# Kernel tuning notes

Measured on AMD Instinct MI355X. Metric: run time of the kernel, lower is better.

The kernel has to match this reference:

```python
import jax, jax.numpy as jnp
import numpy as np

Z_DIM = 64
SEQ_LEN = 100
SEQ_DIM = 32
INPUT_SIZE = 128
H_ENC = 256
H_DEC = 256
BATCH = 2048


def setup_inputs() -> dict:
    key = jax.random.key(0)
    ks = jax.random.split(key, 26)
    w = lambda k, sh: jax.random.normal(k, sh, jnp.float32) * 0.05
    return {
        "x": jax.random.normal(ks[0], (BATCH, SEQ_LEN, SEQ_DIM), jnp.float32),
        "eps": jax.random.normal(ks[1], (BATCH, Z_DIM), jnp.float32),
        "W_ee": w(ks[2], (SEQ_DIM, INPUT_SIZE)), "b_ee": w(ks[3], (INPUT_SIZE,)),
        "Wih_f": w(ks[4], (INPUT_SIZE, 3 * H_ENC)), "Whh_f": w(ks[5], (H_ENC, 3 * H_ENC)),
        "bih_f": w(ks[6], (3 * H_ENC,)), "bhh_f": w(ks[7], (3 * H_ENC,)),
        "Wih_b": w(ks[8], (INPUT_SIZE, 3 * H_ENC)), "Whh_b": w(ks[9], (H_ENC, 3 * H_ENC)),
        "bih_b": w(ks[10], (3 * H_ENC,)), "bhh_b": w(ks[11], (3 * H_ENC,)),
        "W_enc": w(ks[12], (2 * H_ENC, 2 * Z_DIM)), "b_enc": w(ks[13], (2 * Z_DIM,)),
        "W_z2h": w(ks[14], (Z_DIM, H_DEC)), "b_z2h": w(ks[15], (H_DEC,)),
        "W_h2i": w(ks[16], (H_DEC, INPUT_SIZE // 2)), "b_h2i": w(ks[17], (INPUT_SIZE // 2,)),
        "Wih_d": w(ks[18], (INPUT_SIZE, 3 * H_DEC)), "Whh_d": w(ks[19], (H_DEC, 3 * H_DEC)),
        "bih_d": w(ks[20], (3 * H_DEC,)), "bhh_d": w(ks[21], (3 * H_DEC,)),
        "W_ed": w(ks[22], (SEQ_DIM, INPUT_SIZE // 2)), "b_ed": w(ks[23], (INPUT_SIZE // 2,)),
        "W_dec": w(ks[24], (H_DEC, SEQ_DIM)), "b_dec": w(ks[25], (SEQ_DIM,)),
    }


def _gru_cell(x, h, Wih, Whh, bih, bhh):
    # PyTorch GRU cell math (gate order: reset, update, new)
    gi = x @ Wih + bih
    gh = h @ Whh + bhh
    ir, iz, in_ = jnp.split(gi, 3, axis=-1)
    hr, hz, hn = jnp.split(gh, 3, axis=-1)
    r = jax.nn.sigmoid(ir + hr)
    u = jax.nn.sigmoid(iz + hz)
    n = jnp.tanh(in_ + r * hn)
    return (1.0 - u) * n + u * h


def reference(x, eps, W_ee, b_ee, Wih_f, Whh_f, bih_f, bhh_f, Wih_b, Whh_b, bih_b, bhh_b,
              W_enc, b_enc, W_z2h, b_z2h, W_h2i, b_h2i, Wih_d, Whh_d, bih_d, bhh_d,
              W_ed, b_ed, W_dec, b_dec):
    B = x.shape[0]
    # ---- encoder ----
    xe = jax.nn.relu(x @ W_ee + b_ee)  # [B, L, 128]
    h0 = jnp.zeros((B, H_ENC), x.dtype)

    def enc_step(h, xt):
        return _gru_cell(xt, h, Wih_f, Whh_f, bih_f, bhh_f), None

    h_fwd, _ = jax.lax.scan(enc_step, h0, xe.transpose(1, 0, 2))
    # backward direction: only its output at the LAST timestep is used by the
    # original (output[:, -1, :]), which equals a single GRU step on the last
    # input from the zero initial state -> identical math, no wasted scan.
    h_bwd = _gru_cell(xe[:, -1], h0, Wih_b, Whh_b, bih_b, bhh_b)
    stats = jnp.concatenate([h_fwd, h_bwd], axis=-1) @ W_enc + b_enc  # [B, 2z]
    mu, logvar = stats[:, :Z_DIM], stats[:, Z_DIM:]
    z = mu + jnp.exp(logvar * 0.5) * eps
    h_dec0 = jax.nn.relu(z @ W_z2h + b_z2h)           # initial hidden [B, 256]
    hid_inp = jax.nn.relu(h_dec0 @ W_h2i + b_h2i)     # [B, 64]
    cur = jax.nn.relu(jnp.zeros((B, SEQ_DIM), x.dtype) @ W_ed + b_ed)  # zero start token
    inp0 = jnp.concatenate([cur, hid_inp], axis=-1)   # [B, 128]

    def dec_step(carry, _):
        h, inp = carry
        h2 = _gru_cell(inp, h, Wih_d, Whh_d, bih_d, bhh_d)
        x_cur = h2 @ W_dec + b_dec                    # [B, SEQ_DIM]
        nxt = jnp.concatenate([jax.nn.relu(x_cur @ W_ed + b_ed),
                               jax.nn.relu(h2 @ W_h2i + b_h2i)], axis=-1)
        return (h2, nxt), x_cur

    _, xs = jax.lax.scan(dec_step, (h_dec0, inp0), None, length=SEQ_LEN)
    x_recon = xs.transpose(1, 0, 2)                   # [B, L, SEQ_DIM]
    return x_recon, mu, logvar
```

## Files before the change

### kernel.cpp

```cpp
#include <hip/hip_runtime.h>
#include <hip/hip_bf16.h>

typedef __bf16 bf16x8 __attribute__((ext_vector_type(8)));
typedef float  f32x4  __attribute__((ext_vector_type(4)));
typedef unsigned short u16;

#define DEVI __device__ __forceinline__
#define MFMA __builtin_amdgcn_mfma_f32_16x16x32_bf16

DEVI u16 f2bf(float f){
  unsigned u = __builtin_bit_cast(unsigned, f);
  u += 0x7fffu + ((u >> 16) & 1u);
  return (u16)(u >> 16);
}
DEVI float bf2f(u16 h){
  unsigned u = ((unsigned)h) << 16;
  return __builtin_bit_cast(float, u);
}

enum : int {
  OFF_IHF = 0,
  OFF_HHF = 196608,
  OFF_IHB = 589824,
  OFF_IHD = 786432,
  OFF_HHD = 983040,
  OFF_ENC = 1376256,
  OFF_Z2H = 1507328,
  OFF_H2I = 1540096,
  OFF_DEC = 1572864,
  OFF_EE  = 1589248,
  OFF_ED  = 1597440,
  OFF_DE  = 1601536,
  OFF_BDE = 1634304,
  WS_TOTAL = 1634560
};

DEVI void packseg(const float* __restrict__ W, u16* __restrict__ dst, int li, int N, int KT){
  int j = li & 7, l = (li >> 3) & 63, f = li >> 9;
  int kt = f % KT, ntg = f / KT;
  int k = kt * 32 + ((l >> 4) << 3) + j;
  int col = (ntg << 4) + (l & 15);
  dst[li] = f2bf(W[k * N + col]);
}

__global__ void pack_all(const float* Wihf, const float* Whhf, const float* Wihb,
                         const float* Wihd, const float* Whhd, const float* Wenc,
                         const float* Wz2h, const float* Wh2i, const float* Wdec,
                         const float* Wee,  const float* Wed,
                         const float* bed,  const float* bdec, char* ws)
{
  int idx = blockIdx.x * 256 + threadIdx.x;
  if (idx < 98304) { packseg(Wihf, (u16*)(ws+OFF_IHF), idx, 768, 4); return; } idx -= 98304;
  if (idx < 196608){ packseg(Whhf, (u16*)(ws+OFF_HHF), idx, 768, 8); return; } idx -= 196608;
  if (idx < 98304) { packseg(Wihb, (u16*)(ws+OFF_IHB), idx, 768, 4); return; } idx -= 98304;
  if (idx < 98304) { packseg(Wihd, (u16*)(ws+OFF_IHD), idx, 768, 4); return; } idx -= 98304;
  if (idx < 196608){ packseg(Whhd, (u16*)(ws+OFF_HHD), idx, 768, 8); return; } idx -= 196608;
  if (idx < 65536) { packseg(Wenc, (u16*)(ws+OFF_ENC), idx, 128, 16); return; } idx -= 65536;
  if (idx < 16384) { packseg(Wz2h, (u16*)(ws+OFF_Z2H), idx, 256, 2); return; } idx -= 16384;
  if (idx < 16384) { packseg(Wh2i, (u16*)(ws+OFF_H2I), idx, 64, 8); return; } idx -= 16384;
  if (idx < 8192)  { packseg(Wdec, (u16*)(ws+OFF_DEC), idx, 32, 8); return; } idx -= 8192;
  if (idx < 4096)  { packseg(Wee,  (u16*)(ws+OFF_EE),  idx, 128, 1); return; } idx -= 4096;
  if (idx < 2048)  { packseg(Wed,  (u16*)(ws+OFF_ED),  idx, 64, 1); return; } idx -= 2048;
  if (idx < 16384){
    int j = idx & 7, l = (idx >> 3) & 63, f = idx >> 9;
    int kt = f & 7, ntg = f >> 3;
    int k = kt * 32 + ((l >> 4) << 3) + j;
    int col = (ntg << 4) + (l & 15);
    float acc = 0.f;
    for (int m = 0; m < 32; ++m) acc += Wdec[k*32 + m] * Wed[m*64 + col];
    ((u16*)(ws+OFF_DE))[idx] = f2bf(acc);
    return;
  } idx -= 16384;
  if (idx < 64){
    float acc = bed[idx];
    for (int m = 0; m < 32; ++m) acc += bdec[m] * Wed[m*64 + idx];
    ((float*)(ws+OFF_BDE))[idx] = acc;
  }
}

enum : int { RB_A1 = 272, RB_A2 = 528, RB_X = 80 };

DEVI bf16x8 ldF(const char* buf, int row, int kElem, int rowB){
  return *(const bf16x8*)(buf + row * rowB + kElem * 2);
}
DEVI void stBf(char* buf, int row, int col, int rowB, float v){
  *(u16*)(buf + row * rowB + col * 2) = f2bf(v);
}
DEVI bf16x8 gfrag(const u16* P, int ntg, int KT, int kt, int l){
  return *(const bf16x8*)(P + ((size_t)(ntg * KT + kt) * 64 + l) * 8);
}

DEVI float sigm(float x){ return 1.0f / (1.0f + __expf(-x)); }
DEVI float tanh_f(float x){ return 1.0f - 2.0f / (1.0f + __expf(2.0f * x)); }

DEVI void stage_x(const float* __restrict__ xg, int s0, int t, char* Xb, int tid){
  if (tid < 256){
    int s = tid >> 4, d0 = (tid & 15) * 2;
    float2 v = *(const float2*)(xg + (size_t)(s0 + s) * 3200 + t * 32 + d0);
    unsigned pk = (unsigned)f2bf(v.x) | ((unsigned)f2bf(v.y) << 16);
    *(unsigned*)(Xb + s * RB_X + d0 * 2) = pk;
  }
}

DEVI f32x4 gate_rz(const u16* PI, const u16* PH, int G, int l, int cc, int g4,
                   const char* Ab, const bf16x8 a2f[8]){
  bf16x8 w0 = gfrag(PI, G, 4, 0, l), w1 = gfrag(PI, G, 4, 1, l);
  bf16x8 w2 = gfrag(PI, G, 4, 2, l), w3 = gfrag(PI, G, 4, 3, l);
  bf16x8 a0 = ldF(Ab, cc, 0  + g4 * 8, RB_A1);
  bf16x8 a1 = ldF(Ab, cc, 32 + g4 * 8, RB_A1);
  bf16x8 a2 = ldF(Ab, cc, 64 + g4 * 8, RB_A1);
  bf16x8 a3 = ldF(Ab, cc, 96 + g4 * 8, RB_A1);
  f32x4 acc = {0.f, 0.f, 0.f, 0.f};
  acc = MFMA(a0, w0, acc, 0,0,0); acc = MFMA(a1, w1, acc, 0,0,0);
  acc = MFMA(a2, w2, acc, 0,0,0); acc = MFMA(a3, w3, acc, 0,0,0);
  bf16x8 h0 = gfrag(PH, G, 8, 0, l), h1 = gfrag(PH, G, 8, 1, l);
  bf16x8 h2 = gfrag(PH, G, 8, 2, l), h3 = gfrag(PH, G, 8, 3, l);
  acc = MFMA(a2f[0], h0, acc, 0,0,0); acc = MFMA(a2f[1], h1, acc, 0,0,0);
  acc = MFMA(a2f[2], h2, acc, 0,0,0); acc = MFMA(a2f[3], h3, acc, 0,0,0);
  bf16x8 h4 = gfrag(PH, G, 8, 4, l), h5 = gfrag(PH, G, 8, 5, l);
  bf16x8 h6 = gfrag(PH, G, 8, 6, l), h7 = gfrag(PH, G, 8, 7, l);
  acc = MFMA(a2f[4], h4, acc, 0,0,0); acc = MFMA(a2f[5], h5, acc, 0,0,0);
  acc = MFMA(a2f[6], h6, acc, 0,0,0); acc = MFMA(a2f[7], h7, acc, 0,0,0);
  return acc;
}
DEVI f32x4 gate_i(const u16* PI, int G, int l, int cc, int g4, const char* Ab){
  bf16x8 w0 = gfrag(PI, G, 4, 0, l), w1 = gfrag(PI, G, 4, 1, l);
  bf16x8 w2 = gfrag(PI, G, 4, 2, l), w3 = gfrag(PI, G, 4, 3, l);
  bf16x8 a0 = ldF(Ab, cc, 0  + g4 * 8, RB_A1);
  bf16x8 a1 = ldF(Ab, cc, 32 + g4 * 8, RB_A1);
  bf16x8 a2 = ldF(Ab, cc, 64 + g4 * 8, RB_A1);
  bf16x8 a3 = ldF(Ab, cc, 96 + g4 * 8, RB_A1);
  f32x4 acc = {0.f, 0.f, 0.f, 0.f};
  acc = MFMA(a0, w0, acc, 0,0,0); acc = MFMA(a1, w1, acc, 0,0,0);
  acc = MFMA(a2, w2, acc, 0,0,0); acc = MFMA(a3, w3, acc, 0,0,0);
  return acc;
}
DEVI f32x4 gate_h(const u16* PH, int G, int l, const bf16x8 a2f[8]){
  bf16x8 h0 = gfrag(PH, G, 8, 0, l), h1 = gfrag(PH, G, 8, 1, l);
  bf16x8 h2 = gfrag(PH, G, 8, 2, l), h3 = gfrag(PH, G, 8, 3, l);
  f32x4 acc = {0.f, 0.f, 0.f, 0.f};
  acc = MFMA(a2f[0], h0, acc, 0,0,0); acc = MFMA(a2f[1], h1, acc, 0,0,0);
  acc = MFMA(a2f[2], h2, acc, 0,0,0); acc = MFMA(a2f[3], h3, acc, 0,0,0);
  bf16x8 h4 = gfrag(PH, G, 8, 4, l), h5 = gfrag(PH, G, 8, 5, l);
  bf16x8 h6 = gfrag(PH, G, 8, 6, l), h7 = gfrag(PH, G, 8, 7, l);
  acc = MFMA(a2f[4], h4, acc, 0,0,0); acc = MFMA(a2f[5], h5, acc, 0,0,0);
  acc = MFMA(a2f[6], h6, acc, 0,0,0); acc = MFMA(a2f[7], h7, acc, 0,0,0);
  return acc;
}

DEVI void lbar(){
  asm volatile("s_waitcnt lgkmcnt(0)" ::: "memory");
  __builtin_amdgcn_s_barrier();
}

__global__ __launch_bounds__(512, 1) void vae_main(
    const float* __restrict__ x, const float* __restrict__ eps,
    const float* __restrict__ b_ee,
    const float* __restrict__ bih_f, const float* __restrict__ bhh_f,
    const float* __restrict__ bih_b, const float* __restrict__ bhh_b,
    const float* __restrict__ bih_d, const float* __restrict__ bhh_d,
    const float* __restrict__ b_enc, const float* __restrict__ b_z2h,
    const float* __restrict__ b_h2i, const float* __restrict__ b_ed,
    const float* __restrict__ b_dec,
    const char* __restrict__ ws, float* __restrict__ out)
{
  __shared__ __align__(16) char A1[2][16 * RB_A1];
  __shared__ __align__(16) char A2s[16 * RB_A2];
  __shared__ __align__(16) char HBb[16 * RB_A2];
  __shared__ __align__(16) char X0b[2][16 * RB_X];
  __shared__ float ST[16 * 132];
  __shared__ char PAD[94208];

  const int tid = threadIdx.x;
  const int l = tid & 63;
  const int w = tid >> 6;
  const int cc = l & 15;
  const int g4 = l >> 4;
  const int s0 = blockIdx.x * 16;

  if (tid == 0) PAD[0] = 1;

  const u16* PIHF = (const u16*)(ws + OFF_IHF);
  const u16* PHHF = (const u16*)(ws + OFF_HHF);
  const u16* PIHB = (const u16*)(ws + OFF_IHB);
  const u16* PIHD = (const u16*)(ws + OFF_IHD);
  const u16* PHHD = (const u16*)(ws + OFF_HHD);
  const u16* PENC = (const u16*)(ws + OFF_ENC);
  const u16* PZ2H = (const u16*)(ws + OFF_Z2H);
  const u16* PH2I = (const u16*)(ws + OFF_H2I);
  const u16* PDEC = (const u16*)(ws + OFF_DEC);
  const u16* PEE  = (const u16*)(ws + OFF_EE);
  const u16* PDE  = (const u16*)(ws + OFF_DE);

  const f32x4 zf = {0.f, 0.f, 0.f, 0.f};

  const int u0 = 16 * w + cc, u1 = u0 + 128;
  float brj[2], bzj[2], bij[2], bhj[2];
  brj[0] = bih_f[u0] + bhh_f[u0];         brj[1] = bih_f[u1] + bhh_f[u1];
  bzj[0] = bih_f[256+u0] + bhh_f[256+u0]; bzj[1] = bih_f[256+u1] + bhh_f[256+u1];
  bij[0] = bih_f[512+u0];                 bij[1] = bih_f[512+u1];
  bhj[0] = bhh_f[512+u0];                 bhj[1] = bhh_f[512+u1];
  const float beer = b_ee[u0];
  const bf16x8 bEE = gfrag(PEE, w, 1, 0, l);

  float hr[8];
  #pragma unroll
  for (int i = 0; i < 8; ++i) hr[i] = 0.f;

  stage_x(x, s0, 0, X0b[0], tid);
  for (int i = tid; i < 16 * RB_A2 / 4; i += 512) ((unsigned*)A2s)[i] = 0u;
  __syncthreads();
  {
    bf16x8 a = ldF(X0b[0], cc, g4 * 8, RB_X);
    f32x4 xa = MFMA(a, bEE, zf, 0, 0, 0);
    #pragma unroll
    for (int q = 0; q < 4; ++q)
      stBf(A1[0], g4 * 4 + q, u0, RB_A1, fmaxf(xa[q] + beer, 0.f));
  }
  stage_x(x, s0, 1, X0b[1], tid);
  __syncthreads();

  for (int t = 0; t < 100; ++t){
    const char* Ab = A1[t & 1];
    bf16x8 a2f[8];
    #pragma unroll
    for (int kt = 0; kt < 8; ++kt) a2f[kt] = ldF(A2s, cc, kt * 32 + g4 * 8, RB_A2);
    lbar();

    #pragma unroll
    for (int j = 0; j < 2; ++j){
      f32x4 aR = gate_rz(PIHF, PHHF, w + 8*j,      l, cc, g4, Ab, a2f);
      f32x4 aZ = gate_rz(PIHF, PHHF, w + 16 + 8*j, l, cc, g4, Ab, a2f);
      f32x4 aI = gate_i (PIHF,       w + 32 + 8*j, l, cc, g4, Ab);
      f32x4 aH = gate_h (PHHF,       w + 32 + 8*j, l, a2f);
      const int uj = (j == 0) ? u0 : u1;
      #pragma unroll
      for (int q = 0; q < 4; ++q){
        float r  = sigm(aR[q] + brj[j]);
        float zz = sigm(aZ[q] + bzj[j]);
        float n  = tanh_f(aI[q] + bij[j] + r * (aH[q] + bhj[j]));
        float h  = (1.f - zz) * n + zz * hr[j * 4 + q];
        hr[j * 4 + q] = h;
        stBf(A2s, g4 * 4 + q, uj, RB_A2, h);
      }
    }

    if (t < 99){
      bf16x8 a = ldF(X0b[(t + 1) & 1], cc, g4 * 8, RB_X);
      f32x4 xa = MFMA(a, bEE, zf, 0, 0, 0);
      #pragma unroll
      for (int q = 0; q < 4; ++q)
        stBf(A1[(t + 1) & 1], g4 * 4 + q, u0, RB_A1, fmaxf(xa[q] + beer, 0.f));
    }
    if (t < 98) stage_x(x, s0, t + 2, X0b[t & 1], tid);
    lbar();
  }

  {
    bf16x8 b1f[4];
    #pragma unroll
    for (int kt = 0; kt < 4; ++kt) b1f[kt] = ldF(A1[1], cc, kt * 32 + g4 * 8, RB_A1);
    #pragma unroll
    for (int j = 0; j < 2; ++j){
      f32x4 bR = zf, bZ = zf, bI = zf;
      #pragma unroll
      for (int kt = 0; kt < 4; ++kt){
        bR = MFMA(b1f[kt], gfrag(PIHB, w + 8*j,      4, kt, l), bR, 0,0,0);
        bZ = MFMA(b1f[kt], gfrag(PIHB, w + 16 + 8*j, 4, kt, l), bZ, 0,0,0);
        bI = MFMA(b1f[kt], gfrag(PIHB, w + 32 + 8*j, 4, kt, l), bI, 0,0,0);
      }
      const int uj = (j == 0) ? u0 : u1;
      const float brb = bih_b[uj] + bhh_b[uj];
      const float bzb = bih_b[256+uj] + bhh_b[256+uj];
      const float bib = bih_b[512+uj], bhb = bhh_b[512+uj];
      #pragma unroll
      for (int q = 0; q < 4; ++q){
        float r  = sigm(bR[q] + brb);
        float zz = sigm(bZ[q] + bzb);
        float n  = tanh_f(bI[q] + bib + r * bhb);
        stBf(HBb, g4 * 4 + q, uj, RB_A2, (1.f - zz) * n);
      }
    }
  }
  __syncthreads();

  {
    f32x4 sa = zf;
    #pragma unroll
    for (int kt = 0; kt < 8; ++kt)
      sa = MFMA(ldF(A2s, cc, kt * 32 + g4 * 8, RB_A2), gfrag(PENC, w, 16, kt, l), sa, 0, 0, 0);
    #pragma unroll
    for (int kt = 8; kt < 16; ++kt)
      sa = MFMA(ldF(HBb, cc, (kt - 8) * 32 + g4 * 8, RB_A2), gfrag(PENC, w, 16, kt, l), sa, 0, 0, 0);
    const float be = b_enc[16 * w + cc];
    #pragma unroll
    for (int q = 0; q < 4; ++q)
      ST[(g4 * 4 + q) * 132 + 16 * w + cc] = sa[q] + be;
  }
  __syncthreads();

  {
    const int s = tid >> 5, jj = (tid & 31) * 2;
    #pragma unroll
    for (int d = 0; d < 2; ++d){
      const int j = jj + d;
      float mu = ST[s * 132 + j], lv = ST[s * 132 + 64 + j];
      out[6553600u + (size_t)(s0 + s) * 64 + j] = mu;
      out[6684672u + (size_t)(s0 + s) * 64 + j] = lv;
      float zv = mu + __expf(0.5f * lv) * eps[(size_t)(s0 + s) * 64 + j];
      stBf(A1[0], s, j, RB_A1, zv);
    }
  }
  __syncthreads();

  #pragma unroll
  for (int j = 0; j < 2; ++j){
    const int g = w + 8 * j;
    f32x4 da = zf;
    #pragma unroll
    for (int kt = 0; kt < 2; ++kt)
      da = MFMA(ldF(A1[0], cc, kt * 32 + g4 * 8, RB_A1), gfrag(PZ2H, g, 2, kt, l), da, 0, 0, 0);
    const float bz = b_z2h[(j == 0) ? u0 : u1];
    #pragma unroll
    for (int q = 0; q < 4; ++q){
      float v = fmaxf(da[q] + bz, 0.f);
      hr[j * 4 + q] = v;
      stBf(A2s, g4 * 4 + q, (j == 0) ? u0 : u1, RB_A2, v);
    }
  }
  brj[0] = bih_d[u0] + bhh_d[u0];         brj[1] = bih_d[u1] + bhh_d[u1];
  bzj[0] = bih_d[256+u0] + bhh_d[256+u0]; bzj[1] = bih_d[256+u1] + bhh_d[256+u1];
  bij[0] = bih_d[512+u0];                 bij[1] = bih_d[512+u1];
  bhj[0] = bhh_d[512+u0];                 bhj[1] = bhh_d[512+u1];
  __syncthreads();

  const float bh2ir = (w < 4) ? b_h2i[16 * w + cc] : 0.f;
  const float bder  = (w >= 4) ? ((const float*)(ws + OFF_BDE))[16 * (w - 4) + cc] : 0.f;
  const float bdecr = (w == 2 || w == 3) ? b_dec[16 * (w - 2) + cc] : 0.f;

  if (w < 4){
    f32x4 ha = zf;
    #pragma unroll
    for (int kt = 0; kt < 8; ++kt)
      ha = MFMA(ldF(A2s, cc, kt * 32 + g4 * 8, RB_A2), gfrag(PH2I, w, 8, kt, l), ha, 0, 0, 0);
    #pragma unroll
    for (int q = 0; q < 4; ++q)
      stBf(A1[0], g4 * 4 + q, 64 + 16 * w + cc, RB_A1, fmaxf(ha[q] + bh2ir, 0.f));
  }
  {
    const int s = tid >> 5, jj = (tid & 31) * 2;
    #pragma unroll
    for (int d = 0; d < 2; ++d)
      stBf(A1[0], s, jj + d, RB_A1, fmaxf(b_ed[jj + d], 0.f));
  }
  __syncthreads();

  for (int t = 0; t < 100; ++t){
    const char* Ab = A1[0];
    bf16x8 a2f[8];
    #pragma unroll
    for (int kt = 0; kt < 8; ++kt) a2f[kt] = ldF(A2s, cc, kt * 32 + g4 * 8, RB_A2);
    lbar();

    #pragma unroll
    for (int j = 0; j < 2; ++j){
      f32x4 aR = gate_rz(PIHD, PHHD, w + 8*j,      l, cc, g4, Ab, a2f);
      f32x4 aZ = gate_rz(PIHD, PHHD, w + 16 + 8*j, l, cc, g4, Ab, a2f);
      f32x4 aI = gate_i (PIHD,       w + 32 + 8*j, l, cc, g4, Ab);
      f32x4 aH = gate_h (PHHD,       w + 32 + 8*j, l, a2f);
      const int uj = (j == 0) ? u0 : u1;
      #pragma unroll
      for (int q = 0; q < 4; ++q){
        float r  = sigm(aR[q] + brj[j]);
        float zz = sigm(aZ[q] + bzj[j]);
        float n  = tanh_f(aI[q] + bij[j] + r * (aH[q] + bhj[j]));
        float h  = (1.f - zz) * n + zz * hr[j * 4 + q];
        hr[j * 4 + q] = h;
        stBf(A2s, g4 * 4 + q, uj, RB_A2, h);
      }
    }
    lbar();

    {
      bf16x8 af[8];
      #pragma unroll
      for (int kt = 0; kt < 8; ++kt) af[kt] = ldF(A2s, cc, kt * 32 + g4 * 8, RB_A2);
      f32x4 hv = zf;
      if (w < 4){
        #pragma unroll
        for (int kt = 0; kt < 8; ++kt) hv = MFMA(af[kt], gfrag(PH2I, w, 8, kt, l), hv, 0, 0, 0);
        #pragma unroll
        for (int q = 0; q < 4; ++q)
          stBf(A1[0], g4 * 4 + q, 64 + 16 * w + cc, RB_A1, fmaxf(hv[q] + bh2ir, 0.f));
      } else {
        #pragma unroll
        for (int kt = 0; kt < 8; ++kt) hv = MFMA(af[kt], gfrag(PDE, w - 4, 8, kt, l), hv, 0, 0, 0);
        #pragma unroll
        for (int q = 0; q < 4; ++q)
          stBf(A1[0], g4 * 4 + q, 16 * (w - 4) + cc, RB_A1, fmaxf(hv[q] + bder, 0.f));
      }
      if (w == 2 || w == 3){
        f32x4 xc = zf;
        #pragma unroll
        for (int kt = 0; kt < 8; ++kt) xc = MFMA(af[kt], gfrag(PDEC, w - 2, 8, kt, l), xc, 0, 0, 0);
        #pragma unroll
        for (int q = 0; q < 4; ++q)
          out[(size_t)(s0 + g4 * 4 + q) * 3200 + t * 32 + 16 * (w - 2) + cc] = xc[q] + bdecr;
      }
    }
    lbar();
  }
}

extern "C" void kernel_launch(void* const* d_in, const int* in_sizes, int n_in,
                              void* d_out, int out_size, void* d_ws, size_t ws_size,
                              hipStream_t stream)
{
  (void)in_sizes; (void)n_in; (void)out_size;
  if (ws_size < (size_t)WS_TOTAL) return;

  const float* x    = (const float*)d_in[0];
  const float* eps  = (const float*)d_in[1];
  const float* Wee  = (const float*)d_in[2];
  const float* bee  = (const float*)d_in[3];
  const float* Wihf = (const float*)d_in[4];
  const float* Whhf = (const float*)d_in[5];
  const float* bihf = (const float*)d_in[6];
  const float* bhhf = (const float*)d_in[7];
  const float* Wihb = (const float*)d_in[8];
  const float* bihb = (const float*)d_in[10];
  const float* bhhb = (const float*)d_in[11];
  const float* Wenc = (const float*)d_in[12];
  const float* benc = (const float*)d_in[13];
  const float* Wz2h = (const float*)d_in[14];
  const float* bz2h = (const float*)d_in[15];
  const float* Wh2i = (const float*)d_in[16];
  const float* bh2i = (const float*)d_in[17];
  const float* Wihd = (const float*)d_in[18];
  const float* Whhd = (const float*)d_in[19];
  const float* bihd = (const float*)d_in[20];
  const float* bhhd = (const float*)d_in[21];
  const float* Wed  = (const float*)d_in[22];
  const float* bed  = (const float*)d_in[23];
  const float* Wdec = (const float*)d_in[24];
  const float* bdec = (const float*)d_in[25];
  char* ws = (char*)d_ws;

  pack_all<<<3193, 256, 0, stream>>>(Wihf, Whhf, Wihb, Wihd, Whhd, Wenc, Wz2h, Wh2i,
                                     Wdec, Wee, Wed, bed, bdec, ws);
  vae_main<<<128, 512, 0, stream>>>(x, eps, bee, bihf, bhhf, bihb, bhhb, bihd, bhhd,
                                    benc, bz2h, bh2i, bed, bdec, ws, (float*)d_out);
}
```

Measured before the change: 1.188 ms.

## Cache part of GRU weight fragments in LDS via global_load_lds DMA

Each wave preloads a 16KB slice of its recurrent and input weight fragments (reset gate, first z-gate input tile) into a new 128KB shared buffer using direct global-to-LDS loads, once before the encoder and once before the decoder loop. The first gate group then reads B operands from LDS instead of global/L2 every timestep, cutting repeated weight traffic in the latency-bound recurrence. The dummy padding array that previously forced one block per CU is removed, and the HB/ST scratch buffers are aliased into the cache region. The aliasing assumes those scratch uses never overlap with live cached weights.

```diff
diff --git a/kernel.cpp b/kernel.cpp
--- a/kernel.cpp
+++ b/kernel.cpp
@@ -102,6 +102,30 @@
   }
 }
 
+DEVI void dma16(const u16* g, char* lds){
+  __builtin_amdgcn_global_load_lds(
+      (const __attribute__((address_space(1))) unsigned*)(const void*)g,
+      (__attribute__((address_space(3))) unsigned*)(void*)lds, 16, 0, 0);
+}
+DEVI void issue4(const u16* src, char* dst, int l){
+  const u16* g0 = src + l * 8;
+  dma16(g0, dst); dma16(g0 + 512, dst + 1024);
+  dma16(g0 + 1024, dst + 2048); dma16(g0 + 1536, dst + 3072);
+}
+DEVI const u16* srcIH(const u16* PI, int ntg){ return PI + (size_t)ntg * 2048; }
+DEVI const u16* srcHL(const u16* PH, int ntg){ return PH + (size_t)ntg * 4096; }
+DEVI const u16* srcHH(const u16* PH, int ntg){ return PH + (size_t)ntg * 4096 + 2048; }
+DEVI bf16x8 ldS(const char* base, int f, int l){
+  return *(const bf16x8*)(base + f * 1024 + l * 16);
+}
+
+DEVI void fill_cache(const u16* PI, const u16* PH, int w, int l, char* cwb){
+  issue4(srcIH(PI, w),      cwb,         l);
+  issue4(srcHL(PH, w),      cwb + 4096,  l);
+  issue4(srcHH(PH, w),      cwb + 8192,  l);
+  issue4(srcIH(PI, w + 16), cwb + 12288, l);
+}
+
 DEVI f32x4 gate_rz(const u16* PI, const u16* PH, int G, int l, int cc, int g4,
                    const char* Ab, const bf16x8 a2f[8]){
   bf16x8 w0 = gfrag(PI, G, 4, 0, l), w1 = gfrag(PI, G, 4, 1, l);
@@ -123,6 +147,43 @@
   acc = MFMA(a2f[6], h6, acc, 0,0,0); acc = MFMA(a2f[7], h7, acc, 0,0,0);
   return acc;
 }
+DEVI f32x4 gate_r_cached(const char* cwb, int l, int cc, int g4,
+                         const char* Ab, const bf16x8 a2f[8]){
+  bf16x8 a0 = ldF(Ab, cc, 0  + g4 * 8, RB_A1);
+  bf16x8 a1 = ldF(Ab, cc, 32 + g4 * 8, RB_A1);
+  bf16x8 a2 = ldF(Ab, cc, 64 + g4 * 8, RB_A1);
+  bf16x8 a3 = ldF(Ab, cc, 96 + g4 * 8, RB_A1);
+  f32x4 acc = {0.f, 0.f, 0.f, 0.f};
+  acc = MFMA(a0, ldS(cwb, 0, l), acc, 0,0,0);
+  acc = MFMA(a1, ldS(cwb, 1, l), acc, 0,0,0);
+  acc = MFMA(a2, ldS(cwb, 2, l), acc, 0,0,0);
+  acc = MFMA(a3, ldS(cwb, 3, l), acc, 0,0,0);
+  #pragma unroll
+  for (int kt = 0; kt < 8; ++kt)
+    acc = MFMA(a2f[kt], ldS(cwb, 4 + kt, l), acc, 0,0,0);
+  return acc;
+}
+DEVI f32x4 gate_z_cached(const char* cwb, const u16* PH, int G, int l, int cc,
+                         int g4, const char* Ab, const bf16x8 a2f[8]){
+  bf16x8 a0 = ldF(Ab, cc, 0  + g4 * 8, RB_A1);
+  bf16x8 a1 = ldF(Ab, cc, 32 + g4 * 8, RB_A1);
+  bf16x8 a2 = ldF(Ab, cc, 64 + g4 * 8, RB_A1);
+  bf16x8 a3 = ldF(Ab, cc, 96 + g4 * 8, RB_A1);
+  f32x4 acc = {0.f, 0.f, 0.f, 0.f};
+  acc = MFMA(a0, ldS(cwb, 12, l), acc, 0,0,0);
+  acc = MFMA(a1, ldS(cwb, 13, l), acc, 0,0,0);
+  acc = MFMA(a2, ldS(cwb, 14, l), acc, 0,0,0);
+  acc = MFMA(a3, ldS(cwb, 15, l), acc, 0,0,0);
+  bf16x8 h0 = gfrag(PH, G, 8, 0, l), h1 = gfrag(PH, G, 8, 1, l);
+  bf16x8 h2 = gfrag(PH, G, 8, 2, l), h3 = gfrag(PH, G, 8, 3, l);
+  acc = MFMA(a2f[0], h0, acc, 0,0,0); acc = MFMA(a2f[1], h1, acc, 0,0,0);
+  acc = MFMA(a2f[2], h2, acc, 0,0,0); acc = MFMA(a2f[3], h3, acc, 0,0,0);
+  bf16x8 h4 = gfrag(PH, G, 8, 4, l), h5 = gfrag(PH, G, 8, 5, l);
+  bf16x8 h6 = gfrag(PH, G, 8, 6, l), h7 = gfrag(PH, G, 8, 7, l);
+  acc = MFMA(a2f[4], h4, acc, 0,0,0); acc = MFMA(a2f[5], h5, acc, 0,0,0);
+  acc = MFMA(a2f[6], h6, acc, 0,0,0); acc = MFMA(a2f[7], h7, acc, 0,0,0);
+  return acc;
+}
 DEVI f32x4 gate_i(const u16* PI, int G, int l, int cc, int g4, const char* Ab){
   bf16x8 w0 = gfrag(PI, G, 4, 0, l), w1 = gfrag(PI, G, 4, 1, l);
   bf16x8 w2 = gfrag(PI, G, 4, 2, l), w3 = gfrag(PI, G, 4, 3, l);
@@ -164,12 +225,10 @@
     const float* __restrict__ b_dec,
     const char* __restrict__ ws, float* __restrict__ out)
 {
+  __shared__ __align__(16) char CW[131072];
   __shared__ __align__(16) char A1[2][16 * RB_A1];
   __shared__ __align__(16) char A2s[16 * RB_A2];
-  __shared__ __align__(16) char HBb[16 * RB_A2];
   __shared__ __align__(16) char X0b[2][16 * RB_X];
-  __shared__ float ST[16 * 132];
-  __shared__ char PAD[94208];
 
   const int tid = threadIdx.x;
   const int l = tid & 63;
@@ -177,8 +236,6 @@
   const int cc = l & 15;
   const int g4 = l >> 4;
   const int s0 = blockIdx.x * 16;
-
-  if (tid == 0) PAD[0] = 1;
 
   const u16* PIHF = (const u16*)(ws + OFF_IHF);
   const u16* PHHF = (const u16*)(ws + OFF_HHF);
@@ -193,6 +250,9 @@
   const u16* PDE  = (const u16*)(ws + OFF_DE);
 
   const f32x4 zf = {0.f, 0.f, 0.f, 0.f};
+  char* cwb = CW + (size_t)w * 16384;
+  char* HBb = CW;
+  float* ST = (float*)(CW + 16384);
 
   const int u0 = 16 * w + cc, u1 = u0 + 128;
   float brj[2], bzj[2], bij[2], bhj[2];
@@ -209,6 +269,7 @@
 
   stage_x(x, s0, 0, X0b[0], tid);
   for (int i = tid; i < 16 * RB_A2 / 4; i += 512) ((unsigned*)A2s)[i] = 0u;
+  fill_cache(PIHF, PHHF, w, l, cwb);
   __syncthreads();
   {
     bf16x8 a = ldF(X0b[0], cc, g4 * 8, RB_X);
@@ -218,6 +279,7 @@
       stBf(A1[0], g4 * 4 + q, u0, RB_A1, fmaxf(xa[q] + beer, 0.f));
   }
   stage_x(x, s0, 1, X0b[1], tid);
+  asm volatile("s_waitcnt vmcnt(0)" ::: "memory");
   __syncthreads();
 
   for (int t = 0; t < 100; ++t){
@@ -227,21 +289,34 @@
     for (int kt = 0; kt < 8; ++kt) a2f[kt] = ldF(A2s, cc, kt * 32 + g4 * 8, RB_A2);
     lbar();
 
-    #pragma unroll
-    for (int j = 0; j < 2; ++j){
-      f32x4 aR = gate_rz(PIHF, PHHF, w + 8*j,      l, cc, g4, Ab, a2f);
-      f32x4 aZ = gate_rz(PIHF, PHHF, w + 16 + 8*j, l, cc, g4, Ab, a2f);
-      f32x4 aI = gate_i (PIHF,       w + 32 + 8*j, l, cc, g4, Ab);
-      f32x4 aH = gate_h (PHHF,       w + 32 + 8*j, l, a2f);
-      const int uj = (j == 0) ? u0 : u1;
+    {
+      f32x4 aR = gate_r_cached(cwb, l, cc, g4, Ab, a2f);
+      f32x4 aZ = gate_z_cached(cwb, PHHF, w + 16, l, cc, g4, Ab, a2f);
+      f32x4 aI = gate_i (PIHF, w + 32, l, cc, g4, Ab);
+      f32x4 aH = gate_h (PHHF, w + 32, l, a2f);
       #pragma unroll
       for (int q = 0; q < 4; ++q){
-        float r  = sigm(aR[q] + brj[j]);
-        float zz = sigm(aZ[q] + bzj[j]);
-        float n  = tanh_f(aI[q] + bij[j] + r * (aH[q] + bhj[j]));
-        float h  = (1.f - zz) * n + zz * hr[j * 4 + q];
-        hr[j * 4 + q] = h;
-        stBf(A2s, g4 * 4 + q, uj, RB_A2, h);
+        float r  = sigm(aR[q] + brj[0]);
+        float zz = sigm(aZ[q] + bzj[0]);
+        float n  = tanh_f(aI[q] + bij[0] + r * (aH[q] + bhj[0]));
+        float h  = (1.f - zz) * n + zz * hr[q];
+        hr[q] = h;
+        stBf(A2s, g4 * 4 + q, u0, RB_A2, h);
+      }
+    }
+    {
+      f32x4 aR = gate_rz(PIHF, PHHF, w + 8,  l, cc, g4, Ab, a2f);
+      f32x4 aZ = gate_rz(PIHF, PHHF, w + 24, l, cc, g4, Ab, a2f);
+      f32x4 aI = gate_i (PIHF, w + 40, l, cc, g4, Ab);
+      f32x4 aH = gate_h (PHHF, w + 40, l, a2f);
+      #pragma unroll
+      for (int q = 0; q < 4; ++q){
+        float r  = sigm(aR[q] + brj[1]);
+        float zz = sigm(aZ[q] + bzj[1]);
+        float n  = tanh_f(aI[q] + bij[1] + r * (aH[q] + bhj[1]));
+        float h  = (1.f - zz) * n + zz * hr[4 + q];
+        hr[4 + q] = h;
+        stBf(A2s, g4 * 4 + q, u1, RB_A2, h);
       }
     }
 
@@ -313,6 +388,7 @@
   }
   __syncthreads();
 
+  fill_cache(PIHD, PHHD, w, l, cwb);
   #pragma unroll
   for (int j = 0; j < 2; ++j){
     const int g = w + 8 * j;
@@ -353,6 +429,7 @@
     for (int d = 0; d < 2; ++d)
       stBf(A1[0], s, jj + d, RB_A1, fmaxf(b_ed[jj + d], 0.f));
   }
+  asm volatile("s_waitcnt vmcnt(0)" ::: "memory");
   __syncthreads();
 
   for (int t = 0; t < 100; ++t){
@@ -362,21 +439,34 @@
     for (int kt = 0; kt < 8; ++kt) a2f[kt] = ldF(A2s, cc, kt * 32 + g4 * 8, RB_A2);
     lbar();
 
-    #pragma unroll
-    for (int j = 0; j < 2; ++j){
-      f32x4 aR = gate_rz(PIHD, PHHD, w + 8*j,      l, cc, g4, Ab, a2f);
-      f32x4 aZ = gate_rz(PIHD, PHHD, w + 16 + 8*j, l, cc, g4, Ab, a2f);
-      f32x4 aI = gate_i (PIHD,       w + 32 + 8*j, l, cc, g4, Ab);
-      f32x4 aH = gate_h (PHHD,       w + 32 + 8*j, l, a2f);
-      const int uj = (j == 0) ? u0 : u1;
+    {
+      f32x4 aR = gate_r_cached(cwb, l, cc, g4, Ab, a2f);
+      f32x4 aZ = gate_z_cached(cwb, PHHD, w + 16, l, cc, g4, Ab, a2f);
+      f32x4 aI = gate_i (PIHD, w + 32, l, cc, g4, Ab);
+      f32x4 aH = gate_h (PHHD, w + 32, l, a2f);
       #pragma unroll
       for (int q = 0; q < 4; ++q){
-        float r  = sigm(aR[q] + brj[j]);
-        float zz = sigm(aZ[q] + bzj[j]);
-        float n  = tanh_f(aI[q] + bij[j] + r * (aH[q] + bhj[j]));
-        float h  = (1.f - zz) * n + zz * hr[j * 4 + q];
-        hr[j * 4 + q] = h;
-        stBf(A2s, g4 * 4 + q, uj, RB_A2, h);
+        float r  = sigm(aR[q] + brj[0]);
+        float zz = sigm(aZ[q] + bzj[0]);
+        float n  = tanh_f(aI[q] + bij[0] + r * (aH[q] + bhj[0]));
+        float h  = (1.f - zz) * n + zz * hr[q];
+        hr[q] = h;
+        stBf(A2s, g4 * 4 + q, u0, RB_A2, h);
+      }
+    }
+    {
+      f32x4 aR = gate_rz(PIHD, PHHD, w + 8,  l, cc, g4, Ab, a2f);
+      f32x4 aZ = gate_rz(PIHD, PHHD, w + 24, l, cc, g4, Ab, a2f);
+      f32x4 aI = gate_i (PIHD, w + 40, l, cc, g4, Ab);
+      f32x4 aH = gate_h (PHHD, w + 40, l, a2f);
+      #pragma unroll
+      for (int q = 0; q < 4; ++q){
+        float r  = sigm(aR[q] + brj[1]);
+        float zz = sigm(aZ[q] + bzj[1]);
+        float n  = tanh_f(aI[q] + bij[1] + r * (aH[q] + bhj[1]));
+        float h  = (1.f - zz) * n + zz * hr[4 + q];
+        hr[4 + q] = h;
+        stBf(A2s, g4 * 4 + q, u1, RB_A2, h);
       }
     }
     lbar();
```

Result: faster. 1.105 ms (-6.9%).
